# Performance work log

Measured on AMD Instinct MI355X. Metric: run time of the kernel, lower is better.

The kernel has to match this reference:

```python
import jax, jax.numpy as jnp
import numpy as np

B, T, NF, C, H, TOPK = 4, 8, 8192, 384, 12, 32
D = C // H
SCALE = D ** -0.5  # qk_scale=None -> head_dim**-0.5


def setup_inputs() -> dict:
    key = jax.random.key(0)
    ks = jax.random.split(key, 4)
    x = jax.random.normal(ks[0], (B, T + NF, C), jnp.float32)
    qs_w = jax.random.normal(ks[1], (T, C, C), jnp.float32) * (C ** -0.5)
    kv_w = jax.random.normal(ks[2], (C, 2 * C), jnp.float32) * (C ** -0.5)
    experts_w = jax.random.normal(ks[3], (T, C, C), jnp.float32) * (C ** -0.5)
    return {"x": x, "qs_w": qs_w, "kv_w": kv_w, "experts_w": experts_w}


def reference(x, qs_w, kv_w, experts_w):
    # x: [B, T+NF, C]; first T tokens are task tokens, rest are feature tokens
    feature = x[:, T:, :]                                          # [B,NF,C]
    kv = (feature @ kv_w).reshape(B, NF, 2, H, D)                  # out dim splits [2,H,D]
    k = kv[:, :, 0].transpose(0, 2, 1, 3)                          # [B,H,NF,D]
    v = kv[:, :, 1].transpose(0, 2, 1, 3)                          # [B,H,NF,D]
    # per-task query linears (no bias), one task token each
    q = jnp.einsum('btc,tco->bto', x[:, :T, :], qs_w)              # [B,T,C]
    q = q.reshape(B, T, H, D).transpose(0, 2, 1, 3)                # [B,H,T,D]
    attn = jnp.einsum('bhtd,bhnd->bhtn', q, k) * SCALE             # [B,H,T,NF]
    vals, idx = jax.lax.top_k(attn, TOPK)                          # [B,H,T,K]
    w = jax.nn.softmax(vals, axis=-1)                              # softmax over top-k only
    # attn_token = (scatter(topk softmax) @ v) == weighted gather of v rows
    v_g = jnp.take_along_axis(v[:, :, None], idx[..., None], axis=3)   # [B,H,T,K,D]
    attn_token = jnp.einsum('bhtk,bhtkd->bhtd', w, v_g)
    attn_token = attn_token.transpose(0, 2, 1, 3).reshape(B, T, C)     # [B,T,C]
    # gather raw feature tokens at top-k indices, weight, scatter into padded zeros
    fm = feature.reshape(B, NF, H, D).transpose(0, 2, 1, 3)        # [B,H,NF,D]
    f_g = jnp.take_along_axis(fm[:, :, None], idx[..., None], axis=3) * w[..., None]  # [B,H,T,K,D]
    bi = jnp.arange(B)[:, None, None, None]
    hi = jnp.arange(H)[None, :, None, None]
    ti = jnp.arange(T)[None, None, :, None]
    # topk indices are unique per row -> set is well-defined
    feature_pad = jnp.zeros((B, H, T, NF, D), x.dtype).at[bi, hi, ti, idx].set(f_g)
    feature_pad = feature_pad.transpose(0, 2, 3, 1, 4).reshape(B, T, NF, C)  # [B,T,NF,C]
    # per-task expert linears; einsum with ones weight == sum over tasks
    feature_out = jnp.einsum('btnc,tco->bno', feature_pad, experts_w)  # [B,NF,C]
    token_out = jnp.einsum('btc,tco->bto', attn_token, experts_w)      # [B,T,C]
    return jnp.concatenate([token_out, feature_out], axis=1)          # [B,T+NF,C]
```

## Files before the change

kernel.cpp:

```cpp
#include <hip/hip_runtime.h>
#include <hip/hip_bf16.h>
#include <math.h>

#define B 4
#define T 8
#define NF 8192
#define C 384
#define H 12
#define TOPK 32
#define D 32
#define STOT (T + NF)
#define R (H * T)
#define KSEL 48
#define NCH 4
#define CHSZ (NF / NCH)
#define SCALE 0.17677669529663687f

typedef unsigned int uint;
typedef unsigned short ushort;
typedef short bf16x8 __attribute__((ext_vector_type(8)));
typedef float f32x4 __attribute__((ext_vector_type(4)));

__device__ __forceinline__ ushort bf16u(float a) {
  return __builtin_bit_cast(ushort, __float2bfloat16(a));
}
__device__ __forceinline__ float bf16f(ushort u) {
  uint v = (uint)u << 16;
  return __builtin_bit_cast(float, v);
}
__device__ __forceinline__ ushort f32_key(float s) {
  uint kb = bf16u(s);
  kb ^= (kb & 0x8000u) ? 0xFFFFu : 0x8000u;
  return (ushort)kb;
}

__global__ __launch_bounds__(256) void ta_qproj_kernel(
    const float* __restrict__ x, const float* __restrict__ qs_w,
    float* __restrict__ q_part) {
  int t = blockIdx.x;
  int o0 = blockIdx.y * 64;
  int z = blockIdx.z;
  int tid = threadIdx.x;
  int o = tid & 63, ks = tid >> 6;
  __shared__ float xs[B][192];
  __shared__ float part[4][B][64];
  if (tid < 192) {
    int b = tid / 48, j4 = (tid % 48) * 4;
    *reinterpret_cast<float4*>(&xs[b][j4]) =
        *reinterpret_cast<const float4*>(x + ((size_t)b * STOT + t) * C + z * 192 + j4);
  }
  __syncthreads();
  float a0 = 0.f, a1 = 0.f, a2 = 0.f, a3 = 0.f;
  const float* w = qs_w + (size_t)t * C * C + (size_t)(z * 192 + ks * 48) * C + o0 + o;
#pragma unroll 8
  for (int c = 0; c < 48; ++c) {
    float wv = w[(size_t)c * C];
    int cj = ks * 48 + c;
    a0 += xs[0][cj] * wv;
    a1 += xs[1][cj] * wv;
    a2 += xs[2][cj] * wv;
    a3 += xs[3][cj] * wv;
  }
  part[ks][0][o] = a0; part[ks][1][o] = a1;
  part[ks][2][o] = a2; part[ks][3][o] = a3;
  __syncthreads();
  {
    int b = tid >> 6, oo = tid & 63;
    float s = part[0][b][oo] + part[1][b][oo] + part[2][b][oo] + part[3][b][oo];
    q_part[(((size_t)z * B + b) * T + t) * C + o0 + oo] = s;
  }
}

__global__ __launch_bounds__(384) void ta_fold_kernel(
    const float* __restrict__ q_part, const float* __restrict__ kv_w,
    ushort* __restrict__ qk_hi, ushort* __restrict__ qk_lo) {
  int b = blockIdx.x / H, h = blockIdx.x % H;
  int tid = threadIdx.x;
  __shared__ float kS[C][33];
  __shared__ float qh[T][D];
  if (tid < T * D) {
    int t = tid >> 5, d = tid & 31;
    qh[t][d] = q_part[((size_t)b * T + t) * C + h * D + d] +
               q_part[(((size_t)B + b) * T + t) * C + h * D + d];
  }
  for (int j = tid; j < C * 8; j += 384) {
    int c = j >> 3, d4 = (j & 7) * 4;
    float4 v = *reinterpret_cast<const float4*>(
        kv_w + (size_t)c * (2 * C) + h * D + d4);
    kS[c][d4 + 0] = v.x; kS[c][d4 + 1] = v.y;
    kS[c][d4 + 2] = v.z; kS[c][d4 + 3] = v.w;
  }
  __syncthreads();
  float acc[T] = {0.f, 0.f, 0.f, 0.f, 0.f, 0.f, 0.f, 0.f};
#pragma unroll
  for (int d = 0; d < D; ++d) {
    float kv = kS[tid][d];
#pragma unroll
    for (int t = 0; t < T; ++t) acc[t] += qh[t][d] * kv;
  }
#pragma unroll
  for (int t = 0; t < T; ++t) {
    size_t off = ((size_t)b * R + (size_t)h * T + t) * C + tid;
    float a = acc[t];
    ushort hh = bf16u(a);
    qk_hi[off] = hh;
    qk_lo[off] = bf16u(a - bf16f(hh));
  }
}

__global__ __launch_bounds__(256) void ta_scores_kernel(
    const float* __restrict__ x, const ushort* __restrict__ qk_hi,
    const ushort* __restrict__ qk_lo, ushort* __restrict__ keys,
    float* __restrict__ scoresF) {
  int b = blockIdx.y;
  int n0 = blockIdx.x * 64;
  int tid = threadIdx.x;
  int lane = tid & 63, w = tid >> 6;
  int row16 = lane & 15, kg = lane >> 4;
  __shared__ ushort fH[64][72], fL[64][72];
  __shared__ ushort qH[96][72], qL[96][72];
  f32x4 acc[6];
#pragma unroll
  for (int i = 0; i < 6; ++i) acc[i] = (f32x4){0.f, 0.f, 0.f, 0.f};

  const float* xb = x + ((size_t)b * STOT + T + n0) * C;
  const ushort* qhb = qk_hi + (size_t)b * R * C;
  const ushort* qlb = qk_lo + (size_t)b * R * C;

  int frow = tid >> 2, fcg = (tid & 3) * 8;

#pragma unroll 1
  for (int c0 = 0; c0 < C; c0 += 32) {
    {
      const float* src = xb + (size_t)frow * C + c0 + fcg;
      float4 v0 = *reinterpret_cast<const float4*>(src);
      float4 v1 = *reinterpret_cast<const float4*>(src + 4);
      float vv[8] = {v0.x, v0.y, v0.z, v0.w, v1.x, v1.y, v1.z, v1.w};
      ushort hh[8], ll[8];
#pragma unroll
      for (int j = 0; j < 8; ++j) {
        hh[j] = bf16u(vv[j]);
        ll[j] = bf16u(vv[j] - bf16f(hh[j]));
      }
      uint4 ph, pl;
      ph.x = (uint)hh[0] | ((uint)hh[1] << 16);
      ph.y = (uint)hh[2] | ((uint)hh[3] << 16);
      ph.z = (uint)hh[4] | ((uint)hh[5] << 16);
      ph.w = (uint)hh[6] | ((uint)hh[7] << 16);
      pl.x = (uint)ll[0] | ((uint)ll[1] << 16);
      pl.y = (uint)ll[2] | ((uint)ll[3] << 16);
      pl.z = (uint)ll[4] | ((uint)ll[5] << 16);
      pl.w = (uint)ll[6] | ((uint)ll[7] << 16);
      *reinterpret_cast<uint4*>(&fH[frow][fcg]) = ph;
      *reinterpret_cast<uint4*>(&fL[frow][fcg]) = pl;
    }
#pragma unroll
    for (int s = 0; s < 3; ++s) {
      int u = tid + 256 * s;
      int v = (u >= 384) ? u - 384 : u;
      int row = v >> 2, cg = (v & 3) * 8;
      if (u < 384) {
        uint4 t4 = *reinterpret_cast<const uint4*>(qhb + (size_t)row * C + c0 + cg);
        *reinterpret_cast<uint4*>(&qH[row][cg]) = t4;
      } else {
        uint4 t4 = *reinterpret_cast<const uint4*>(qlb + (size_t)row * C + c0 + cg);
        *reinterpret_cast<uint4*>(&qL[row][cg]) = t4;
      }
    }
    __syncthreads();
    bf16x8 bh = *reinterpret_cast<const bf16x8*>(&fH[w * 16 + row16][kg * 8]);
    bf16x8 bl = *reinterpret_cast<const bf16x8*>(&fL[w * 16 + row16][kg * 8]);
#pragma unroll
    for (int i = 0; i < 6; ++i) {
      bf16x8 ah = *reinterpret_cast<const bf16x8*>(&qH[i * 16 + row16][kg * 8]);
      bf16x8 al = *reinterpret_cast<const bf16x8*>(&qL[i * 16 + row16][kg * 8]);
      acc[i] = __builtin_amdgcn_mfma_f32_16x16x32_bf16(ah, bh, acc[i], 0, 0, 0);
      acc[i] = __builtin_amdgcn_mfma_f32_16x16x32_bf16(ah, bl, acc[i], 0, 0, 0);
      acc[i] = __builtin_amdgcn_mfma_f32_16x16x32_bf16(al, bh, acc[i], 0, 0, 0);
    }
    __syncthreads();
  }
  int n = n0 + w * 16 + row16;
#pragma unroll
  for (int i = 0; i < 6; ++i) {
    int rbase = i * 16 + kg * 4;
#pragma unroll
    for (int reg = 0; reg < 4; ++reg) {
      float s = acc[i][reg] * SCALE;
      size_t off = ((size_t)b * R + rbase + reg) * NF + n;
      keys[off] = f32_key(s);
      scoresF[off] = s;
    }
  }
}

__global__ __launch_bounds__(256) void ta_selchunk_kernel(
    const ushort* __restrict__ keys, uint* __restrict__ cand_buf,
    float4* __restrict__ out4) {
  int ch = blockIdx.x, rr = blockIdx.y;
  int tid = threadIdx.x;
  int lane = tid & 63, wvi = tid >> 6;
  __shared__ uint hist[4096];
  __shared__ uint cand[CHSZ];
  __shared__ uint wtot[4];
  __shared__ uint sh_piv, cnt;
  const ushort* kp = keys + (size_t)rr * NF + (size_t)ch * CHSZ;

  {
    float4 z = {0.f, 0.f, 0.f, 0.f};
    float4* dst = out4 + (size_t)(rr * NCH + ch) * 2050;
    for (int j = tid; j < 2050; j += 256) dst[j] = z;
  }

  {
    uint4 z4 = {0u, 0u, 0u, 0u};
    uint4* hz = reinterpret_cast<uint4*>(hist);
    for (int i = tid; i < 1024; i += 256) hz[i] = z4;
  }
  if (tid == 0) cnt = 0;
  __syncthreads();
  for (int i = tid; i < CHSZ; i += 256) atomicAdd(&hist[kp[i] >> 4], 1u);
  __syncthreads();

  uint pp = 0;
#pragma unroll
  for (int j = 0; j < 16; ++j) pp += hist[tid * 16 + j];
  uint suf = pp;
#pragma unroll
  for (int off = 1; off < 64; off <<= 1) {
    uint o = __shfl_down(suf, off);
    if (lane + off < 64) suf += o;
  }
  if (lane == 0) wtot[wvi] = suf;
  __syncthreads();
  {
    uint later = 0;
    for (int wq = wvi + 1; wq < 4; ++wq) later += wtot[wq];
    uint geg = later + suf;
    uint gng = geg - pp;
    if (geg >= (uint)KSEL && gng < (uint)KSEL) {
      uint run = gng;
      int pv = 0;
      for (int j = 15; j >= 0; --j) {
        uint c = hist[tid * 16 + j];
        uint nrun = run + c;
        if (nrun >= (uint)KSEL && run < (uint)KSEL) pv = tid * 16 + j;
        run = nrun;
      }
      sh_piv = (uint)pv;
    }
  }
  __syncthreads();
  uint piv = sh_piv;
  for (int i = tid; i < CHSZ; i += 256) {
    uint u = kp[i];
    if ((u >> 4) >= piv) {
      uint s = atomicAdd(&cnt, 1u);
      cand[s] = (u << 13) | (8191u - (uint)(ch * CHSZ + i));
    }
  }
  __syncthreads();
  uint m = cnt;
  for (int i2 = tid; i2 < (int)m; i2 += 256) {
    uint me = cand[i2];
    int r = 0;
    for (uint e = 0; e < m; ++e) r += (cand[e] > me);
    if (r < KSEL) cand_buf[((size_t)rr * NCH + ch) * KSEL + r] = me;
  }
}

__global__ __launch_bounds__(384) void ta_mergetail_kernel(
    const uint* __restrict__ cand_buf, const float* __restrict__ scoresF,
    const float* __restrict__ x, const float* __restrict__ kv_w,
    const float* __restrict__ ew, float* __restrict__ out) {
  constexpr int M = NCH * KSEL;
  int rr = blockIdx.x;
  int t = rr % T, h = (rr / T) % H, b = rr / R;
  int hD = h * D;
  int tid = threadIdx.x;
  __shared__ float sfS[M];
  __shared__ int idxS[M];
  __shared__ float wl[TOPK];
  __shared__ int top_il[TOPK];
  __shared__ float fbarS[C];
  __shared__ float gS[TOPK][D];
  __shared__ float part[8][D];
  __shared__ __align__(16) float attS[D];
  __shared__ float smax, esum;

  if (tid < M) {
    uint me = cand_buf[(size_t)rr * M + tid];
    int idx = 8191 - (int)(me & 8191u);
    idxS[tid] = idx;
    sfS[tid] = scoresF[(size_t)rr * NF + idx];
  }
  __syncthreads();
  if (tid < M) {
    float mys = sfS[tid];
    int myn = idxS[tid];
    int r = 0;
#pragma unroll 8
    for (int e = 0; e < M; ++e) {
      float se = sfS[e];
      r += (se > mys) || (se == mys && idxS[e] < myn);
    }
    if (r < TOPK) { wl[r] = mys; top_il[r] = myn; }
    if (r == 0) smax = mys;
  }
  __syncthreads();
  {
    float e = 0.f;
    if (tid < TOPK) e = expf(wl[tid] - smax);
    if (tid < 64) {
      float t2 = e;
#pragma unroll
      for (int off = 32; off; off >>= 1) t2 += __shfl_down(t2, off);
      if (tid == 0) esum = t2;
    }
    __syncthreads();
    if (tid < TOPK) wl[tid] = e / esum;
  }
  __syncthreads();

  {
    float fbar = 0.f;
    bool ing = (tid >= hD) && (tid < hD + D);
#pragma unroll 4
    for (int k = 0; k < TOPK; ++k) {
      float v = x[((size_t)b * STOT + T + top_il[k]) * C + tid];
      float wv = wl[k] * v;
      fbar += wv;
      if (ing) gS[k][tid - hD] = wv;
    }
    fbarS[tid] = fbar;
  }
  __syncthreads();

  if (tid < 256) {
    int d = tid & 31, seg = tid >> 5;
    const float* vw = kv_w + C + hD + d;
    float a0 = 0.f, a1 = 0.f;
    int cb = seg * 48;
#pragma unroll 8
    for (int c = 0; c < 48; c += 2) {
      a0 += fbarS[cb + c] * vw[(size_t)(cb + c) * (2 * C)];
      a1 += fbarS[cb + c + 1] * vw[(size_t)(cb + c + 1) * (2 * C)];
    }
    part[seg][d] = a0 + a1;
  }
  __syncthreads();
  if (tid < D) {
    float a = 0.f;
#pragma unroll
    for (int s = 0; s < 8; ++s) a += part[s][tid];
    attS[tid] = a;
  }
  __syncthreads();

  float ewc[D];
  const float* ewt = ew + (size_t)t * C * C + (size_t)hD * C + tid;
#pragma unroll
  for (int dd = 0; dd < D; ++dd) ewc[dd] = ewt[(size_t)dd * C];
  size_t obase = (size_t)b * STOT * C + tid;
#pragma unroll 1
  for (int kk = 0; kk < TOPK; ++kk) {
    float y = 0.f;
#pragma unroll
    for (int d4 = 0; d4 < D; d4 += 4) {
      float4 g4 = *reinterpret_cast<const float4*>(&gS[kk][d4]);
      y += g4.x * ewc[d4] + g4.y * ewc[d4 + 1] +
           g4.z * ewc[d4 + 2] + g4.w * ewc[d4 + 3];
    }
    atomicAdd(&out[obase + (size_t)(T + top_il[kk]) * C], y);
  }
  {
    float y = 0.f;
#pragma unroll
    for (int d4 = 0; d4 < D; d4 += 4) {
      float4 a4 = *reinterpret_cast<const float4*>(attS + d4);
      y += a4.x * ewc[d4] + a4.y * ewc[d4 + 1] +
           a4.z * ewc[d4 + 2] + a4.w * ewc[d4 + 3];
    }
    atomicAdd(&out[obase + (size_t)t * C], y);
  }
}

extern "C" void kernel_launch(void* const* d_in, const int* in_sizes, int n_in,
                              void* d_out, int out_size, void* d_ws, size_t ws_size,
                              hipStream_t stream) {
  const float* x = (const float*)d_in[0];
  const float* qs_w = (const float*)d_in[1];
  const float* kv_w = (const float*)d_in[2];
  const float* ew = (const float*)d_in[3];
  float* out = (float*)d_out;

  char* p = (char*)d_ws;
  ushort* qk_hi = (ushort*)p;  p += (size_t)B * R * C * 2;
  ushort* qk_lo = (ushort*)p;  p += (size_t)B * R * C * 2;
  ushort* keys = (ushort*)p;   p += (size_t)B * R * NF * 2;
  float* scoresF = (float*)p;  p += (size_t)B * R * NF * 4;
  uint* cand_buf = (uint*)p;   p += (size_t)B * R * NCH * KSEL * 4;
  float* q_part = (float*)p;

  dim3 gq(T, C / 64, 2);
  ta_qproj_kernel<<<gq, 256, 0, stream>>>(x, qs_w, q_part);
  ta_fold_kernel<<<B * H, 384, 0, stream>>>(q_part, kv_w, qk_hi, qk_lo);
  dim3 g2(NF / 64, B);
  ta_scores_kernel<<<g2, 256, 0, stream>>>(x, qk_hi, qk_lo, keys, scoresF);
  dim3 gs(NCH, B * R);
  ta_selchunk_kernel<<<gs, 256, 0, stream>>>(keys, cand_buf, (float4*)out);
  ta_mergetail_kernel<<<B * R, 384, 0, stream>>>(cand_buf, scoresF, x, kv_w, ew, out);
}
```

Baseline: 88.63 us.

## Split merge and tail into separate kernels, quartering top-k work per tail block

```diff
diff --git a/kernel.cpp b/kernel.cpp
--- a/kernel.cpp
+++ b/kernel.cpp
@@ -269,33 +269,26 @@
   }
 }
 
-__global__ __launch_bounds__(384) void ta_mergetail_kernel(
+__global__ __launch_bounds__(192) void ta_merge_kernel(
     const uint* __restrict__ cand_buf, const float* __restrict__ scoresF,
-    const float* __restrict__ x, const float* __restrict__ kv_w,
-    const float* __restrict__ ew, float* __restrict__ out) {
+    float* __restrict__ w_buf, int* __restrict__ idx_buf) {
   constexpr int M = NCH * KSEL;
   int rr = blockIdx.x;
-  int t = rr % T, h = (rr / T) % H, b = rr / R;
-  int hD = h * D;
   int tid = threadIdx.x;
   __shared__ float sfS[M];
   __shared__ int idxS[M];
-  __shared__ float wl[TOPK];
-  __shared__ int top_il[TOPK];
-  __shared__ float fbarS[C];
-  __shared__ float gS[TOPK][D];
-  __shared__ float part[8][D];
-  __shared__ __align__(16) float attS[D];
-  __shared__ float smax, esum;
-
-  if (tid < M) {
+  __shared__ float wlS[TOPK];
+  __shared__ int ilS[TOPK];
+  __shared__ float esum;
+
+  {
     uint me = cand_buf[(size_t)rr * M + tid];
     int idx = 8191 - (int)(me & 8191u);
     idxS[tid] = idx;
     sfS[tid] = scoresF[(size_t)rr * NF + idx];
   }
   __syncthreads();
-  if (tid < M) {
+  {
     float mys = sfS[tid];
     int myn = idxS[tid];
     int r = 0;
@@ -304,13 +297,11 @@
       float se = sfS[e];
       r += (se > mys) || (se == mys && idxS[e] < myn);
     }
-    if (r < TOPK) { wl[r] = mys; top_il[r] = myn; }
-    if (r == 0) smax = mys;
-  }
-  __syncthreads();
-  {
-    float e = 0.f;
-    if (tid < TOPK) e = expf(wl[tid] - smax);
+    if (r < TOPK) { wlS[r] = mys; ilS[r] = myn; }
+  }
+  __syncthreads();
+  {
+    float e = (tid < TOPK) ? expf(wlS[tid] - wlS[0]) : 0.f;
     if (tid < 64) {
       float t2 = e;
 #pragma unroll
@@ -318,16 +309,41 @@
       if (tid == 0) esum = t2;
     }
     __syncthreads();
-    if (tid < TOPK) wl[tid] = e / esum;
+    if (tid < TOPK) {
+      w_buf[(size_t)rr * TOPK + tid] = expf(wlS[tid] - wlS[0]) / esum;
+      idx_buf[(size_t)rr * TOPK + tid] = ilS[tid];
+    }
+  }
+}
+
+__global__ __launch_bounds__(384) void ta_tail_kernel(
+    const float* __restrict__ x, const float* __restrict__ kv_w,
+    const float* __restrict__ ew, const float* __restrict__ w_buf,
+    const int* __restrict__ idx_buf, float* __restrict__ out) {
+  constexpr int KQ = TOPK / 4;
+  int q = blockIdx.x & 3, rr = blockIdx.x >> 2;
+  int t = rr % T, h = (rr / T) % H, b = rr / R;
+  int hD = h * D;
+  int tid = threadIdx.x;
+  __shared__ float wl[KQ];
+  __shared__ int il[KQ];
+  __shared__ float fbarS[C];
+  __shared__ float gS[KQ][D];
+  __shared__ float part[8][D];
+  __shared__ __align__(16) float attS[D];
+
+  if (tid < KQ) {
+    wl[tid] = w_buf[(size_t)rr * TOPK + q * KQ + tid];
+    il[tid] = idx_buf[(size_t)rr * TOPK + q * KQ + tid];
   }
   __syncthreads();
 
   {
     float fbar = 0.f;
     bool ing = (tid >= hD) && (tid < hD + D);
-#pragma unroll 4
-    for (int k = 0; k < TOPK; ++k) {
-      float v = x[((size_t)b * STOT + T + top_il[k]) * C + tid];
+#pragma unroll
+    for (int k = 0; k < KQ; ++k) {
+      float v = x[((size_t)b * STOT + T + il[k]) * C + tid];
       float wv = wl[k] * v;
       fbar += wv;
       if (ing) gS[k][tid - hD] = wv;
@@ -363,7 +379,7 @@
   for (int dd = 0; dd < D; ++dd) ewc[dd] = ewt[(size_t)dd * C];
   size_t obase = (size_t)b * STOT * C + tid;
 #pragma unroll 1
-  for (int kk = 0; kk < TOPK; ++kk) {
+  for (int kk = 0; kk < KQ; ++kk) {
     float y = 0.f;
 #pragma unroll
     for (int d4 = 0; d4 < D; d4 += 4) {
@@ -371,7 +387,7 @@
       y += g4.x * ewc[d4] + g4.y * ewc[d4 + 1] +
            g4.z * ewc[d4 + 2] + g4.w * ewc[d4 + 3];
     }
-    atomicAdd(&out[obase + (size_t)(T + top_il[kk]) * C], y);
+    atomicAdd(&out[obase + (size_t)(T + il[kk]) * C], y);
   }
   {
     float y = 0.f;
@@ -400,6 +416,8 @@
   ushort* keys = (ushort*)p;   p += (size_t)B * R * NF * 2;
   float* scoresF = (float*)p;  p += (size_t)B * R * NF * 4;
   uint* cand_buf = (uint*)p;   p += (size_t)B * R * NCH * KSEL * 4;
+  float* w_buf = (float*)p;    p += (size_t)B * R * TOPK * 4;
+  int* idx_buf = (int*)p;      p += (size_t)B * R * TOPK * 4;
   float* q_part = (float*)p;
 
   dim3 gq(T, C / 64, 2);
@@ -409,5 +427,6 @@
   ta_scores_kernel<<<g2, 256, 0, stream>>>(x, qk_hi, qk_lo, keys, scoresF);
   dim3 gs(NCH, B * R);
   ta_selchunk_kernel<<<gs, 256, 0, stream>>>(keys, cand_buf, (float4*)out);
-  ta_mergetail_kernel<<<B * R, 384, 0, stream>>>(cand_buf, scoresF, x, kv_w, ew, out);
-}
+  ta_merge_kernel<<<B * R, 192, 0, stream>>>(cand_buf, scoresF, w_buf, idx_buf);
+  ta_tail_kernel<<<4 * B * R, 384, 0, stream>>>(x, kv_w, ew, w_buf, idx_buf, out);
+}
```

Result: no change. 88.10 us (-0.6%).
